# Optimization experiments

Measured on AMD Instinct MI355X. Metric: run time of the kernel, lower is better.

Reference implementation:

```python
import jax, jax.numpy as jnp
import numpy as np

TAU_MIN, TAU_MAX, TAU_SMALL, N_REF = 0.005, 0.1, 0.3, 4


def _l2norm(x, eps=1e-12):
    # matches torch F.normalize: x / max(||x||_2, eps)
    n = jnp.linalg.norm(x, axis=-1, keepdims=True)
    return x / jnp.maximum(n, eps)


def setup_inputs() -> dict:
    key = jax.random.key(0)
    k1, k2, k3 = jax.random.split(key, 3)
    B, C, H, W = 8, 384, 40, 40
    feats = jax.random.normal(k1, (B, C, H, W), dtype=jnp.float32)
    refs = jax.random.normal(k2, (N_REF, B, C, H, W), dtype=jnp.float32)
    sopm = jax.random.uniform(k3, (B, 1, 160, 160), dtype=jnp.float32)
    log_tau = jnp.array([np.log(0.03)], dtype=jnp.float32)
    alpha_raw = jnp.array([0.0], dtype=jnp.float32)
    return {"feats": feats, "refs": refs, "sopm": sopm,
            "log_tau": log_tau, "alpha_raw": alpha_raw}


def reference(feats, refs, sopm, log_tau, alpha_raw):
    B, C, H, W = feats.shape
    N = H * W
    # buffer contents and SOPM cache are detached in the torch module
    refs = jax.lax.stop_gradient(refs)
    sopm = jax.lax.stop_gradient(sopm)

    tau = jnp.clip(jnp.exp(log_tau[0]), TAU_MIN, TAU_MAX)
    alpha = jax.nn.sigmoid(alpha_raw[0])

    tokens = feats.reshape(B, C, N).transpose(0, 2, 1)   # [B, N, C]
    cur_n = _l2norm(tokens)

    n_ref = refs.shape[0]
    warped_sum = jnp.zeros_like(tokens)
    for r in range(n_ref):  # fixed small ref-frame loop (n_ref=4)
        ref_tok = refs[r].reshape(B, C, N).transpose(0, 2, 1)  # [B, N, C]
        ref_n = _l2norm(ref_tok)
        sim = jnp.einsum('bnc,bmc->bnm', cur_n, ref_n)          # cosine sims
        w = jax.nn.softmax(sim / tau, axis=-1)                  # [B, N, N]
        warped_sum = warped_sum + jnp.einsum('bnm,bmc->bnc', w, ref_tok)
    warped = warped_sum / n_ref

    # SOPM(t-1) -> bilinear resize (align_corners=False) -> threshold mask
    sopm_r = jax.image.resize(sopm, (B, 1, H, W), method='bilinear')
    mask = (sopm_r.reshape(B, 1, N).transpose(0, 2, 1) > TAU_SMALL).astype(feats.dtype)  # [B,N,1]

    alpha_eff = alpha  # full buffer: n_avail == n_ref
    fused = alpha_eff * warped + (1.0 - alpha_eff) * tokens
    enhanced = mask * fused + (1.0 - mask) * tokens
    return enhanced.transpose(0, 2, 1).reshape(B, C, H, W)
```

## Files before the change

kernel.cpp:

```cpp
#include <hip/hip_runtime.h>
#include <stdint.h>

#define B_  8
#define C_  384
#define N_  1600
#define R_  4
#define S_  160
#define HW_ 40

typedef float  f32x4  __attribute__((ext_vector_type(4)));
typedef __bf16 bf16x8 __attribute__((ext_vector_type(8)));
typedef long long i64t;

__device__ __forceinline__ unsigned short f2bf(float x){
  __bf16 h = (__bf16)x;
  return __builtin_bit_cast(unsigned short, h);
}
__device__ __forceinline__ float bf2f(unsigned short u){
  return __builtin_bit_cast(float, (uint32_t)u << 16);
}
__device__ __forceinline__ uint32_t pk_fp8x4(float a, float b, float c, float d){
  int lo = __builtin_amdgcn_cvt_pk_fp8_f32(a, b, 0, false);
  int hi = __builtin_amdgcn_cvt_pk_fp8_f32(c, d, 0, false);
  return (uint32_t)(lo & 0xffff) | ((uint32_t)hi << 16);
}

__device__ __forceinline__ void gload_lds16(const void* g, void* l){
  __builtin_amdgcn_global_load_lds(
      (const __attribute__((address_space(1))) uint32_t*)g,
      (__attribute__((address_space(3))) uint32_t*)l, 16, 0, 0);
}

__global__ void prep_kernel(const float* __restrict__ feats,
                            const float* __restrict__ refs,
                            unsigned char* __restrict__ Qb,
                            unsigned char* __restrict__ Kb,
                            unsigned short* __restrict__ Vb){
  int nt = blockIdx.x, mat = blockIdx.y;
  __shared__ unsigned short tile[64][386];
  __shared__ float ssp[64][17];
  __shared__ float inv_sh[64];
  int t = threadIdx.x;
  bool isref = (mat >= B_);
  const float* src = isref ? refs  + (size_t)(mat - B_) * C_ * N_
                           : feats + (size_t)mat * C_ * N_;
  int n4  = t & 15;
  int crb = t >> 4;
  float ss4[4] = {0.f, 0.f, 0.f, 0.f};
#pragma unroll
  for (int ct = 0; ct < 6; ++ct){
#pragma unroll
    for (int i = 0; i < 4; ++i){
      int c = ct * 64 + crb + 16 * i;
      size_t off = (size_t)c * N_ + nt * 64 + n4 * 4;
      float4 v = *(const float4*)(src + off);
      ushort4 o;
      o.x = f2bf(v.x); o.y = f2bf(v.y); o.z = f2bf(v.z); o.w = f2bf(v.w);
      if (isref){
        unsigned short* vdst = Vb + (size_t)(mat - B_) * C_ * N_;
        *(ushort4*)(vdst + off) = o;
      }
      tile[n4*4+0][c] = o.x;
      tile[n4*4+1][c] = o.y;
      tile[n4*4+2][c] = o.z;
      tile[n4*4+3][c] = o.w;
      ss4[0] += v.x * v.x;  ss4[1] += v.y * v.y;
      ss4[2] += v.z * v.z;  ss4[3] += v.w * v.w;
    }
  }
#pragma unroll
  for (int j = 0; j < 4; ++j) ssp[n4*4+j][crb] = ss4[j];
  __syncthreads();
  if (t < 64){
    float s = 0.f;
#pragma unroll
    for (int p = 0; p < 16; ++p) s += ssp[t][p];
    inv_sh[t] = 1.f / fmaxf(sqrtf(s), 1e-12f);
  }
  __syncthreads();
  unsigned char* dst = isref ? Kb + (size_t)(mat - B_) * N_ * C_
                             : Qb + (size_t)mat * N_ * C_;
#pragma unroll
  for (int i = 0; i < 4; ++i){
    int nr = (t >> 4) + 16 * i;
    float iv = inv_sh[nr];
    unsigned char* drow = dst + (size_t)(nt * 64 + nr) * C_;
#pragma unroll
    for (int ct = 0; ct < 6; ++ct){
      int c0 = ct * 64 + (t & 15) * 4;
      uint32_t a0 = *(const uint32_t*)(&tile[nr][c0]);
      uint32_t a1 = *(const uint32_t*)(&tile[nr][c0 + 2]);
      uint32_t pk = pk_fp8x4(bf2f((unsigned short)(a0 & 0xffff)) * iv,
                             bf2f((unsigned short)(a0 >> 16))    * iv,
                             bf2f((unsigned short)(a1 & 0xffff)) * iv,
                             bf2f((unsigned short)(a1 >> 16))    * iv);
      *(uint32_t*)(drow + c0) = pk;
    }
  }
}

__global__ void mask_kernel(const float* __restrict__ sopm,
                            float* __restrict__ maskp){
  int gid = blockIdx.x * 256 + threadIdx.x;
  int b = gid / N_, n = gid - b * N_;
  int oy = n / HW_, ox = n - oy * HW_;
  const float* sp = sopm + (size_t)b * S_ * S_;
  float cy = oy * 4 + 1.5f, cx = ox * 4 + 1.5f;
  int y0 = 4*oy - 2; if (y0 < 0) y0 = 0;
  int y1 = 4*oy + 5; if (y1 > S_-1) y1 = S_-1;
  int x0 = 4*ox - 2; if (x0 < 0) x0 = 0;
  int x1 = 4*ox + 5; if (x1 > S_-1) x1 = S_-1;
  float wsy = 0.f, wsx = 0.f;
  for (int j = y0; j <= y1; ++j) wsy += 1.f - fabsf(j - cy) * 0.25f;
  for (int j = x0; j <= x1; ++j) wsx += 1.f - fabsf(j - cx) * 0.25f;
  float acc = 0.f;
  for (int jy = y0; jy <= y1; ++jy){
    float wy = 1.f - fabsf(jy - cy) * 0.25f;
    float rs = 0.f;
    for (int jx = x0; jx <= x1; ++jx)
      rs += (1.f - fabsf(jx - cx) * 0.25f) * sp[jy * S_ + jx];
    acc += wy * rs;
  }
  float val = acc / (wsy * wsx);
  maskp[gid] = (val > 0.3f) ? 1.f : 0.f;
}

#define KB0_   0
#define KB1_   12288
#define VB_    24576
#define P_OFF  49152
#define LDS_SZ 53248

__global__ __launch_bounds__(256, 2) void attn_kernel(
    const unsigned char* __restrict__ Qb,
    const unsigned char* __restrict__ Kb,
    const unsigned short* __restrict__ Vb,
    const float* __restrict__ log_tau,
    unsigned short* __restrict__ Or)
{
  __shared__ __align__(16) char lds[LDS_SZ];
  int wg   = blockIdx.x;
  int orig = (wg & 7) * 100 + (wg >> 3);
  int qt   = orig % 25;
  int rb   = orig / 25;
  int b    = rb & 7;
  int tid  = threadIdx.x;
  int lane = tid & 63;
  int w    = tid >> 6;
  int mw   = w >> 1;
  int qw   = w & 1;
  int l15  = lane & 15;
  int lg   = lane >> 4;

  float tau = expf(log_tau[0]);
  tau = fminf(fmaxf(tau, 0.005f), 0.1f);
  float sc = 1.4426950408889634f / tau;

  i64t qreg[2][12];
#pragma unroll
  for (int qt2 = 0; qt2 < 2; ++qt2){
    const unsigned char* qp = Qb +
        ((size_t)b * N_ + qt * 64 + qw * 32 + qt2 * 16 + l15) * C_ + lg * 8;
#pragma unroll
    for (int ks = 0; ks < 12; ++ks)
      qreg[qt2][ks] = *(const i64t*)(qp + ks * 32);
  }

  f32x4 o[4][6];
#pragma unroll
  for (int i = 0; i < 4; ++i)
#pragma unroll
    for (int j = 0; j < 6; ++j) o[i][j] = (f32x4){0.f,0.f,0.f,0.f};
  float lsum0 = 0.f, lsum1 = 0.f;

  const unsigned char*  kmat = Kb + (size_t)rb * N_ * C_;
  const unsigned short* vmat = Vb + (size_t)rb * C_ * N_;
  char* Pb = lds + P_OFF;

  int koffB[3];
#pragma unroll
  for (int i = 0; i < 3; ++i){
    int L = (w * 3 + i) * 64 + lane;
    int m   = L / 24;
    int pos = L - m * 24;
    int cc  = (pos >> 3) * 8 + ((pos & 7) ^ (m & 7));
    koffB[i] = m * C_ + cc * 16;
  }
  int voff[6];
#pragma unroll
  for (int i = 0; i < 6; ++i){
    int chunk = (w * 6 + i) * 64 + lane;
    int line = chunk >> 3;
    int u    = (chunk & 7) ^ (line & 7);
    voff[i]  = (line * 2 + (u >> 2)) * N_ + (u & 3) * 8;
  }

  const int s_l  = (l15 >> 1) & 3;
  const int p_w0 = (qw*32      + l15) * 64 + (((2*mw + (lg >> 1)) ^ s_l) << 4) + (lg & 1) * 8;
  const int p_w1 = (qw*32 + 16 + l15) * 64 + (((2*mw + (lg >> 1)) ^ s_l) << 4) + (lg & 1) * 8;
  const int p_rc = ((lg ^ s_l) << 4) + l15 * 64;

  auto stageK = [&](int t, int buf){
    const unsigned char* kb = kmat + (size_t)t * 32 * C_;
    char* kdst = lds + (buf ? KB1_ : KB0_) + w * 3072;
#pragma unroll
    for (int i = 0; i < 3; ++i) gload_lds16(kb + koffB[i], kdst + i * 1024);
  };
  auto stageV = [&](int t){
    const unsigned short* vb = vmat + t * 32;
    char* vdst = lds + VB_ + w * 6144;
#pragma unroll
    for (int i = 0; i < 6; ++i) gload_lds16(vb + voff[i], vdst + i * 1024);
  };
  const int krow = (mw * 16 + l15);
  auto computeQK = [&](const char* kbR, f32x4& a0acc, f32x4& a1acc){
#pragma unroll
    for (int ks = 0; ks < 12; ++ks){
      int lc  = 2 * ks + (lg >> 1);
      int off = ((lc >> 3) * 8 + ((lc & 7) ^ (krow & 7))) * 16 + (lg & 1) * 8;
      i64t a = *(const i64t*)(kbR + krow * 384 + off);
      a0acc = __builtin_amdgcn_mfma_f32_16x16x32_fp8_fp8(a, qreg[0][ks], a0acc, 0, 0, 0);
      a1acc = __builtin_amdgcn_mfma_f32_16x16x32_fp8_fp8(a, qreg[1][ks], a1acc, 0, 0, 0);
    }
  };

  stageK(0, 0);
  stageV(0);
  stageK(1, 1);
  asm volatile("s_waitcnt vmcnt(9)" ::: "memory");
  __builtin_amdgcn_sched_barrier(0);
  __builtin_amdgcn_s_barrier();
  __builtin_amdgcn_sched_barrier(0);

  f32x4 s0 = {0.f,0.f,0.f,0.f}, s1 = {0.f,0.f,0.f,0.f};
  computeQK(lds + KB0_, s0, s1);

  for (int mt = 0; mt < 50; ++mt){
    int cur = mt & 1;

    ushort4 pw0, pw1;
    {
      __bf16 h;
      float l0 = 0.f, l1 = 0.f;
      h = (__bf16)exp2f((s0[0]-1.f)*sc); l0 += (float)h; pw0.x = __builtin_bit_cast(unsigned short, h);
      h = (__bf16)exp2f((s0[1]-1.f)*sc); l0 += (float)h; pw0.y = __builtin_bit_cast(unsigned short, h);
      h = (__bf16)exp2f((s0[2]-1.f)*sc); l0 += (float)h; pw0.z = __builtin_bit_cast(unsigned short, h);
      h = (__bf16)exp2f((s0[3]-1.f)*sc); l0 += (float)h; pw0.w = __builtin_bit_cast(unsigned short, h);
      h = (__bf16)exp2f((s1[0]-1.f)*sc); l1 += (float)h; pw1.x = __builtin_bit_cast(unsigned short, h);
      h = (__bf16)exp2f((s1[1]-1.f)*sc); l1 += (float)h; pw1.y = __builtin_bit_cast(unsigned short, h);
      h = (__bf16)exp2f((s1[2]-1.f)*sc); l1 += (float)h; pw1.z = __builtin_bit_cast(unsigned short, h);
      h = (__bf16)exp2f((s1[3]-1.f)*sc); l1 += (float)h; pw1.w = __builtin_bit_cast(unsigned short, h);
      lsum0 += l0; lsum1 += l1;
    }
    *(ushort4*)(Pb + p_w0) = pw0;
    *(ushort4*)(Pb + p_w1) = pw1;
    asm volatile("s_waitcnt lgkmcnt(0) vmcnt(0)" ::: "memory");
    __builtin_amdgcn_sched_barrier(0);
    __builtin_amdgcn_s_barrier();
    __builtin_amdgcn_sched_barrier(0);

    if (mt + 2 < 50) stageK(mt + 2, cur);
    __builtin_amdgcn_sched_barrier(0);

    bf16x8 pa[4];
#pragma unroll
    for (int qf2 = 0; qf2 < 4; ++qf2)
      pa[qf2] = *(const bf16x8*)(Pb + qf2 * 1024 + p_rc);
    __builtin_amdgcn_s_setprio(1);
    if (mt + 1 < 50){
      s0 = (f32x4){0.f,0.f,0.f,0.f};
      s1 = (f32x4){0.f,0.f,0.f,0.f};
      computeQK(lds + ((cur ^ 1) ? KB1_ : KB0_), s0, s1);
    }
#pragma unroll
    for (int cf = 0; cf < 6; ++cf){
      int c  = w * 96 + cf * 16 + l15;
      int vo = (c >> 1) * 128 + (((lg | ((c & 1) << 2)) ^ ((c >> 1) & 7)) << 4);
      bf16x8 vf = *(const bf16x8*)(lds + VB_ + vo);
#pragma unroll
      for (int qf2 = 0; qf2 < 4; ++qf2)
        o[qf2][cf] = __builtin_amdgcn_mfma_f32_16x16x32_bf16(pa[qf2], vf, o[qf2][cf], 0, 0, 0);
    }
    __builtin_amdgcn_s_setprio(0);

    __builtin_amdgcn_sched_barrier(0);
    __builtin_amdgcn_s_barrier();
    __builtin_amdgcn_sched_barrier(0);

    if (mt + 1 < 50) stageV(mt + 1);
    __builtin_amdgcn_sched_barrier(0);
  }

  lsum0 += __shfl_xor(lsum0, 16, 64);
  lsum0 += __shfl_xor(lsum0, 32, 64);
  lsum1 += __shfl_xor(lsum1, 16, 64);
  lsum1 += __shfl_xor(lsum1, 32, 64);
  __syncthreads();
  float* lsh = (float*)lds;
  if (lg == 0){
    lsh[mw * 64 + qw * 32 + l15]      = lsum0;
    lsh[mw * 64 + qw * 32 + 16 + l15] = lsum1;
  }
  __syncthreads();
  float invl[4][4];
#pragma unroll
  for (int qf2 = 0; qf2 < 4; ++qf2)
#pragma unroll
    for (int rg = 0; rg < 4; ++rg){
      int q = qf2 * 16 + lg * 4 + rg;
      invl[qf2][rg] = 1.f / (lsh[q] + lsh[64 + q]);
    }

  int qbase = qt * 64;
  unsigned short* op = Or + ((size_t)rb * N_ + qbase) * C_ + w * 96 + l15;
#pragma unroll
  for (int qf2 = 0; qf2 < 4; ++qf2){
#pragma unroll
    for (int cf = 0; cf < 6; ++cf){
#pragma unroll
      for (int rg = 0; rg < 4; ++rg){
        int q = qf2 * 16 + lg * 4 + rg;
        op[(size_t)q * C_ + cf * 16] = f2bf(o[qf2][cf][rg] * invl[qf2][rg]);
      }
    }
  }
}

__global__ void combine_kernel(const unsigned short* __restrict__ Or,
                               const float* __restrict__ feats,
                               const float* __restrict__ maskp,
                               const float* __restrict__ alpha_raw,
                               float* __restrict__ out){
  int nt = blockIdx.x, ct = blockIdx.y, b = blockIdx.z;
  __shared__ float tile[64][65];
  float alpha = 1.f / (1.f + expf(-alpha_raw[0]));
  int t = threadIdx.x;
#pragma unroll
  for (int i = 0; i < 4; ++i){
    int chunk = t + 256 * i;
    int nr = chunk >> 4, c4 = chunk & 15;
    size_t base = ((size_t)b * N_ + nt * 64 + nr) * C_ + ct * 64 + c4 * 4;
    float4 s = {0.f,0.f,0.f,0.f};
#pragma unroll
    for (int r = 0; r < 4; ++r){
      ushort4 v = *(const ushort4*)(Or + (size_t)r * B_ * N_ * C_ + base);
      s.x += bf2f(v.x); s.y += bf2f(v.y); s.z += bf2f(v.z); s.w += bf2f(v.w);
    }
    tile[nr][c4*4+0] = s.x; tile[nr][c4*4+1] = s.y;
    tile[nr][c4*4+2] = s.z; tile[nr][c4*4+3] = s.w;
  }
  __syncthreads();
#pragma unroll
  for (int i = 0; i < 4; ++i){
    int chunk = t + 256 * i;
    int cr = chunk >> 4, n4 = chunk & 15;
    size_t fb = ((size_t)b * C_ + ct * 64 + cr) * N_ + nt * 64 + n4 * 4;
    float4 f  = *(const float4*)(feats + fb);
    float4 mk = *(const float4*)(maskp + (size_t)b * N_ + nt * 64 + n4 * 4);
    float4 ov;
    ov.x = f.x + mk.x * alpha * (tile[n4*4+0][cr] * 0.25f - f.x);
    ov.y = f.y + mk.y * alpha * (tile[n4*4+1][cr] * 0.25f - f.y);
    ov.z = f.z + mk.z * alpha * (tile[n4*4+2][cr] * 0.25f - f.z);
    ov.w = f.w + mk.w * alpha * (tile[n4*4+3][cr] * 0.25f - f.w);
    *(float4*)(out + fb) = ov;
  }
}

__global__ void poison_kernel(float* out, int n){
  int i = blockIdx.x * 256 + threadIdx.x;
  if (i < n) out[i] = 1.0e6f;
}

extern "C" void kernel_launch(void* const* d_in, const int* in_sizes, int n_in,
                              void* d_out, int out_size, void* d_ws, size_t ws_size,
                              hipStream_t stream){
  const float* feats     = (const float*)d_in[0];
  const float* refs      = (const float*)d_in[1];
  const float* sopm      = (const float*)d_in[2];
  const float* log_tau   = (const float*)d_in[3];
  const float* alpha_raw = (const float*)d_in[4];
  float* out = (float*)d_out;

  const size_t SZ_MASK = (size_t)B_ * N_ * 4;
  const size_t SZ_QB   = (size_t)B_ * N_ * C_;
  const size_t SZ_KB   = (size_t)R_ * B_ * N_ * C_;
  const size_t SZ_VB   = (size_t)R_ * B_ * N_ * C_ * 2;
  const size_t SZ_OR   = (size_t)R_ * B_ * N_ * C_ * 2;
  const size_t need = SZ_MASK + SZ_QB + SZ_KB + SZ_VB + SZ_OR;

  if (ws_size < need){
    poison_kernel<<<(out_size + 255) / 256, 256, 0, stream>>>(out, out_size);
    return;
  }
  char* ws = (char*)d_ws;
  float*          maskp = (float*)ws;
  unsigned char*  Qb    = (unsigned char*)(ws + SZ_MASK);
  unsigned char*  Kb    = (unsigned char*)(ws + SZ_MASK + SZ_QB);
  unsigned short* Vb    = (unsigned short*)(ws + SZ_MASK + SZ_QB + SZ_KB);
  unsigned short* Or    = (unsigned short*)(ws + SZ_MASK + SZ_QB + SZ_KB + SZ_VB);

  mask_kernel   <<<50, 256, 0, stream>>>(sopm, maskp);
  prep_kernel   <<<dim3(25, 40), 256, 0, stream>>>(feats, refs, Qb, Kb, Vb);
  attn_kernel   <<<800, 256, 0, stream>>>(Qb, Kb, Vb, log_tau, Or);
  combine_kernel<<<dim3(25, 6, 8), 256, 0, stream>>>(Or, feats, maskp, alpha_raw, out);
}
```

Before: 198.9 us.

## Double-buffer V and P tiles to cut one barrier per attention iteration

The attention loop now keeps two LDS buffers each for the V tile and the softmax probability tile, so the next V load and the next P write no longer conflict with the current PV MMA reads. This drops one of the two workgroup barriers per iteration. It also moves the exp/softmax for the next tile after the PV MMAs, so it runs in software-pipelined fashion. LDS use grows from about 52 KB to 80 KB per block, which could limit how many blocks fit per CU given launch_bounds(256,2).

```diff
diff --git a/kernel.cpp b/kernel.cpp
--- a/kernel.cpp
+++ b/kernel.cpp
@@ -127,9 +127,11 @@
 
 #define KB0_   0
 #define KB1_   12288
-#define VB_    24576
-#define P_OFF  49152
-#define LDS_SZ 53248
+#define VB0_   24576
+#define VB1_   49152
+#define PB0_   73728
+#define PB1_   77824
+#define LDS_SZ 81920
 
 __global__ __launch_bounds__(256, 2) void attn_kernel(
     const unsigned char* __restrict__ Qb,
@@ -175,7 +177,6 @@
 
   const unsigned char*  kmat = Kb + (size_t)rb * N_ * C_;
   const unsigned short* vmat = Vb + (size_t)rb * C_ * N_;
-  char* Pb = lds + P_OFF;
 
   int koffB[3];
 #pragma unroll
@@ -206,9 +207,9 @@
 #pragma unroll
     for (int i = 0; i < 3; ++i) gload_lds16(kb + koffB[i], kdst + i * 1024);
   };
-  auto stageV = [&](int t){
+  auto stageV = [&](int t, int buf){
     const unsigned short* vb = vmat + t * 32;
-    char* vdst = lds + VB_ + w * 6144;
+    char* vdst = lds + (buf ? VB1_ : VB0_) + w * 6144;
 #pragma unroll
     for (int i = 0; i < 6; ++i) gload_lds16(vb + voff[i], vdst + i * 1024);
   };
@@ -225,21 +226,66 @@
   };
 
   stageK(0, 0);
-  stageV(0);
-  stageK(1, 1);
-  asm volatile("s_waitcnt vmcnt(9)" ::: "memory");
+  stageV(0, 0);
+  asm volatile("s_waitcnt vmcnt(0)" ::: "memory");
   __builtin_amdgcn_sched_barrier(0);
   __builtin_amdgcn_s_barrier();
   __builtin_amdgcn_sched_barrier(0);
-
-  f32x4 s0 = {0.f,0.f,0.f,0.f}, s1 = {0.f,0.f,0.f,0.f};
-  computeQK(lds + KB0_, s0, s1);
+  stageK(1, 1);
+  {
+    f32x4 s0 = {0.f,0.f,0.f,0.f}, s1 = {0.f,0.f,0.f,0.f};
+    computeQK(lds + KB0_, s0, s1);
+    ushort4 pw0, pw1;
+    __bf16 h;
+    float l0 = 0.f, l1 = 0.f;
+    h = (__bf16)exp2f((s0[0]-1.f)*sc); l0 += (float)h; pw0.x = __builtin_bit_cast(unsigned short, h);
+    h = (__bf16)exp2f((s0[1]-1.f)*sc); l0 += (float)h; pw0.y = __builtin_bit_cast(unsigned short, h);
+    h = (__bf16)exp2f((s0[2]-1.f)*sc); l0 += (float)h; pw0.z = __builtin_bit_cast(unsigned short, h);
+    h = (__bf16)exp2f((s0[3]-1.f)*sc); l0 += (float)h; pw0.w = __builtin_bit_cast(unsigned short, h);
+    h = (__bf16)exp2f((s1[0]-1.f)*sc); l1 += (float)h; pw1.x = __builtin_bit_cast(unsigned short, h);
+    h = (__bf16)exp2f((s1[1]-1.f)*sc); l1 += (float)h; pw1.y = __builtin_bit_cast(unsigned short, h);
+    h = (__bf16)exp2f((s1[2]-1.f)*sc); l1 += (float)h; pw1.z = __builtin_bit_cast(unsigned short, h);
+    h = (__bf16)exp2f((s1[3]-1.f)*sc); l1 += (float)h; pw1.w = __builtin_bit_cast(unsigned short, h);
+    lsum0 += l0; lsum1 += l1;
+    *(ushort4*)(lds + PB0_ + p_w0) = pw0;
+    *(ushort4*)(lds + PB0_ + p_w1) = pw1;
+  }
+  asm volatile("s_waitcnt lgkmcnt(0) vmcnt(0)" ::: "memory");
+  __builtin_amdgcn_sched_barrier(0);
+  __builtin_amdgcn_s_barrier();
+  __builtin_amdgcn_sched_barrier(0);
 
   for (int mt = 0; mt < 50; ++mt){
     int cur = mt & 1;
 
-    ushort4 pw0, pw1;
-    {
+    if (mt + 1 < 50) stageV(mt + 1, cur ^ 1);
+    if (mt + 2 < 50) stageK(mt + 2, cur);
+    __builtin_amdgcn_sched_barrier(0);
+
+    bf16x8 pa[4];
+    const char* pbR = lds + (cur ? PB1_ : PB0_);
+#pragma unroll
+    for (int qf2 = 0; qf2 < 4; ++qf2)
+      pa[qf2] = *(const bf16x8*)(pbR + qf2 * 1024 + p_rc);
+
+    f32x4 s0 = {0.f,0.f,0.f,0.f}, s1 = {0.f,0.f,0.f,0.f};
+    __builtin_amdgcn_s_setprio(1);
+    if (mt + 1 < 50)
+      computeQK(lds + ((cur ^ 1) ? KB1_ : KB0_), s0, s1);
+    const char* vbR = lds + (cur ? VB1_ : VB0_);
+#pragma unroll
+    for (int cf = 0; cf < 6; ++cf){
+      int c  = w * 96 + cf * 16 + l15;
+      int vo = (c >> 1) * 128 + (((lg | ((c & 1) << 2)) ^ ((c >> 1) & 7)) << 4);
+      bf16x8 vf = *(const bf16x8*)(vbR + vo);
+#pragma unroll
+      for (int qf2 = 0; qf2 < 4; ++qf2)
+        o[qf2][cf] = __builtin_amdgcn_mfma_f32_16x16x32_bf16(pa[qf2], vf, o[qf2][cf], 0, 0, 0);
+    }
+    __builtin_amdgcn_s_setprio(0);
+
+    if (mt + 1 < 50){
+      ushort4 pw0, pw1;
       __bf16 h;
       float l0 = 0.f, l1 = 0.f;
       h = (__bf16)exp2f((s0[0]-1.f)*sc); l0 += (float)h; pw0.x = __builtin_bit_cast(unsigned short, h);
@@ -251,43 +297,14 @@
       h = (__bf16)exp2f((s1[2]-1.f)*sc); l1 += (float)h; pw1.z = __builtin_bit_cast(unsigned short, h);
       h = (__bf16)exp2f((s1[3]-1.f)*sc); l1 += (float)h; pw1.w = __builtin_bit_cast(unsigned short, h);
       lsum0 += l0; lsum1 += l1;
-    }
-    *(ushort4*)(Pb + p_w0) = pw0;
-    *(ushort4*)(Pb + p_w1) = pw1;
+      char* pbW = lds + ((cur ^ 1) ? PB1_ : PB0_);
+      *(ushort4*)(pbW + p_w0) = pw0;
+      *(ushort4*)(pbW + p_w1) = pw1;
+    }
+
     asm volatile("s_waitcnt lgkmcnt(0) vmcnt(0)" ::: "memory");
     __builtin_amdgcn_sched_barrier(0);
     __builtin_amdgcn_s_barrier();
-    __builtin_amdgcn_sched_barrier(0);
-
-    if (mt + 2 < 50) stageK(mt + 2, cur);
-    __builtin_amdgcn_sched_barrier(0);
-
-    bf16x8 pa[4];
-#pragma unroll
-    for (int qf2 = 0; qf2 < 4; ++qf2)
-      pa[qf2] = *(const bf16x8*)(Pb + qf2 * 1024 + p_rc);
-    __builtin_amdgcn_s_setprio(1);
-    if (mt + 1 < 50){
-      s0 = (f32x4){0.f,0.f,0.f,0.f};
-      s1 = (f32x4){0.f,0.f,0.f,0.f};
-      computeQK(lds + ((cur ^ 1) ? KB1_ : KB0_), s0, s1);
-    }
-#pragma unroll
-    for (int cf = 0; cf < 6; ++cf){
-      int c  = w * 96 + cf * 16 + l15;
-      int vo = (c >> 1) * 128 + (((lg | ((c & 1) << 2)) ^ ((c >> 1) & 7)) << 4);
-      bf16x8 vf = *(const bf16x8*)(lds + VB_ + vo);
-#pragma unroll
-      for (int qf2 = 0; qf2 < 4; ++qf2)
-        o[qf2][cf] = __builtin_amdgcn_mfma_f32_16x16x32_bf16(pa[qf2], vf, o[qf2][cf], 0, 0, 0);
-    }
-    __builtin_amdgcn_s_setprio(0);
-
-    __builtin_amdgcn_sched_barrier(0);
-    __builtin_amdgcn_s_barrier();
-    __builtin_amdgcn_sched_barrier(0);
-
-    if (mt + 1 < 50) stageV(mt + 1);
     __builtin_amdgcn_sched_barrier(0);
   }
 
```

Result: faster. 194.4 us (-2.3%).
